# Optimization experiments

Measured on AMD Instinct MI355X. Metric: run time of the kernel, lower is better.

The kernel has to match this reference:

```python
import jax, jax.numpy as jnp
import numpy as np
from jax import lax

N, C_IN, L, K, C_OUT, PAD = 16, 64, 8192, 3, 64, 1

def setup_inputs() -> dict:
    key = jax.random.key(0)
    k1, k2, k3 = jax.random.split(key, 3)
    x = jax.random.normal(k1, (N, C_IN, L), dtype=jnp.float32)
    # kaiming normal (relu): std = sqrt(2 / fan_in), fan_in = C_in * kernel_size
    std_off = np.sqrt(2.0 / (C_IN * K)).astype(np.float32)
    w_off = jax.random.normal(k2, (2 * K, C_IN, K), dtype=jnp.float32) * std_off
    b_off = jnp.zeros((2 * K,), dtype=jnp.float32)
    # 1x1 conv: fan_in = C_in * K (kernel_size 1)
    std_w = np.sqrt(2.0 / (C_IN * K)).astype(np.float32)
    w = jax.random.normal(k3, (C_OUT, C_IN * K), dtype=jnp.float32) * std_w
    b = jnp.zeros((C_OUT,), dtype=jnp.float32)
    return {"x": x, "w_off": w_off, "b_off": b_off, "w": w, "b": b}

def reference(x, w_off, b_off, w, b):
    n, c, l = x.shape
    # offset conv: Conv1d(C, 2K, K, stride=1, padding=PAD)
    offsets = lax.conv_general_dilated(
        x, w_off, window_strides=(1,), padding=[(PAD, PAD)],
        dimension_numbers=("NCH", "OIH", "NCH")) + b_off[None, :, None]
    l_out = offsets.shape[2]
    # [N, 2K, L] -> [N, K, 2, L] -> [N, L, K, 2]; only component 0 is used
    off = offsets.reshape(n, K, 2, l_out).transpose(0, 3, 1, 2)[..., 0]  # [N, L, K]
    x_pad = jnp.pad(x, ((0, 0), (0, 0), (PAD, PAD)))
    lp = l + 2 * PAD
    base = jnp.arange(PAD, lp - PAD, dtype=x.dtype)[None, :, None]  # [1, L, 1]
    grid = jnp.clip(base + off, 0.0, lp - 1)                        # [N, L, K]
    left = jnp.floor(grid).astype(jnp.int32)
    right = jnp.minimum(left + 1, lp - 1)
    alpha = grid - left.astype(x.dtype)                              # [N, L, K]
    idx_l = left.reshape(n, -1)
    idx_r = right.reshape(n, -1)
    gather = jax.vmap(lambda xp, i: xp[:, i])  # per-sample gather over length axis
    x_left = gather(x_pad, idx_l).reshape(n, c, l_out, K)
    x_right = gather(x_pad, idx_r).reshape(n, c, l_out, K)
    a = alpha[:, None]  # [N, 1, L, K]
    x_deform = (1.0 - a) * x_left + a * x_right                      # [N, C, L, K]
    # replicate torch's permute(0,3,2,1).view(N, C*K, L) exactly (row-major)
    x_deform = x_deform.transpose(0, 3, 2, 1).reshape(n, c * K, l_out)
    out = jnp.einsum("om,nml->nol", w, x_deform) + b[None, :, None]
    return out
```

## Files before the change

kernel.cpp:

```cpp
#include <hip/hip_runtime.h>
#include <hip/hip_bf16.h>
#include <math.h>

#define NB   16
#define CIN  64
#define LEN  8192
#define LP2  8195
#define COUT 64
#define MSZ  192

typedef float  f32x4  __attribute__((ext_vector_type(4)));
typedef short  bf16x8 __attribute__((ext_vector_type(8)));

static __device__ inline unsigned short f2bf(float f) {
    __hip_bfloat16 h = __float2bfloat16(f);
    return *reinterpret_cast<unsigned short*>(&h);
}

__global__ __launch_bounds__(256) void prep_kernel(
    const float* __restrict__ x, const float* __restrict__ w_off,
    const float* __restrict__ b_off, const float* __restrict__ w,
    float* __restrict__ gbuf, unsigned int* __restrict__ xt32,
    unsigned short* __restrict__ wtf)
{
    int bid = blockIdx.x;
    int tid = threadIdx.x;

    if (bid >= NB * 128) {
        int b = bid - NB * 128;
        int ot = b / 6, ks = b - ot * 6;
        #pragma unroll
        for (int h = 0; h < 2; ++h) {
            int t2 = tid + h * 256;
            int lq = t2 >> 3, s = t2 & 7;
            int o = ot * 16 + (lq & 15);
            int m = ks * 32 + (lq >> 4) * 8 + s;
            wtf[b * 512 + t2] = f2bf(w[o * MSZ + m]);
        }
        return;
    }

    __shared__ float ps[4][3][64];
    __shared__ unsigned int bt[64 * 33];

    int lane = tid & 63;
    int wid  = __builtin_amdgcn_readfirstlane(tid >> 6);
    int n  = bid >> 7;
    int t  = bid & 127;
    int l0 = t << 6;
    int l  = l0 + lane;
    const float* xn = x + (size_t)n * (CIN * LEN);
    bool okm = (l >= 1);
    bool okp = (l < LEN - 1);

    float a0 = 0.f, a1 = 0.f, a2 = 0.f;
    unsigned int pk[8];

    #pragma unroll
    for (int ci = 0; ci < 16; ci += 2) {
        int c0 = (wid << 4) | ci;
        const float* xc0 = xn + (size_t)c0 * LEN;
        const float* xc1 = xc0 + LEN;
        float xm0 = okm ? xc0[l - 1] : 0.f;
        float x00 = xc0[l];
        float xp0 = okp ? xc0[l + 1] : 0.f;
        float xm1 = okm ? xc1[l - 1] : 0.f;
        float x01 = xc1[l];
        float xp1 = okp ? xc1[l + 1] : 0.f;
        const float* wa = w_off + (size_t)c0 * 3;
        const float* wb = wa + 384;
        const float* wc = wa + 768;
        a0 = fmaf(wa[0], xm0, a0); a0 = fmaf(wa[1], x00, a0); a0 = fmaf(wa[2], xp0, a0);
        a0 = fmaf(wa[3], xm1, a0); a0 = fmaf(wa[4], x01, a0); a0 = fmaf(wa[5], xp1, a0);
        a1 = fmaf(wb[0], xm0, a1); a1 = fmaf(wb[1], x00, a1); a1 = fmaf(wb[2], xp0, a1);
        a1 = fmaf(wb[3], xm1, a1); a1 = fmaf(wb[4], x01, a1); a1 = fmaf(wb[5], xp1, a1);
        a2 = fmaf(wc[0], xm0, a2); a2 = fmaf(wc[1], x00, a2); a2 = fmaf(wc[2], xp0, a2);
        a2 = fmaf(wc[3], xm1, a2); a2 = fmaf(wc[4], x01, a2); a2 = fmaf(wc[5], xp1, a2);
        pk[ci >> 1] = ((unsigned int)f2bf(x01) << 16) | f2bf(x00);
    }

    ps[wid][0][lane] = a0;
    ps[wid][1][lane] = a1;
    ps[wid][2][lane] = a2;
    #pragma unroll
    for (int j = 0; j < 8; ++j)
        bt[lane * 33 + (wid << 3) + j] = pk[j];
    __syncthreads();

    if (tid < 192) {
        int k = tid >> 6, ll = tid & 63;
        float s = b_off[2 * k];
        #pragma unroll
        for (int w4 = 0; w4 < 4; ++w4) s += ps[w4][k][ll];
        float g = fminf(fmaxf((float)(l0 + ll + 1) + s, 0.f), 8193.f);
        gbuf[((size_t)n * LEN + l0 + ll) * 3 + k] = g;
    }

    {
        int row = tid >> 2, grp = tid & 3;
        const unsigned int* src = &bt[row * 33 + (grp << 3)];
        uint4 u0, u1;
        u0.x = src[0]; u0.y = src[1]; u0.z = src[2]; u0.w = src[3];
        u1.x = src[4]; u1.y = src[5]; u1.z = src[6]; u1.w = src[7];
        size_t base = ((size_t)n * LP2 + 1 + l0 + row) * 32 + (grp << 3);
        *(uint4*)&xt32[base]     = u0;
        *(uint4*)&xt32[base + 4] = u1;
    }
    if (t == 0   && tid < 32) xt32[((size_t)n * LP2) * 32 + tid] = 0u;
    if (t == 127 && tid < 64) xt32[((size_t)n * LP2 + 8193 + (tid >> 5)) * 32 + (tid & 31)] = 0u;
}

__global__ __launch_bounds__(256) void dconv6_kernel(
    const unsigned short* __restrict__ xt16, const unsigned short* __restrict__ wtf,
    const float* __restrict__ bias, const float* __restrict__ gbuf,
    float* __restrict__ out)
{
    __shared__ unsigned short Bl[MSZ * 64];
    __shared__ __align__(16) int2 meta[MSZ];
    int tid = threadIdx.x;

    int wg  = blockIdx.x;
    int xcd = wg & 7;
    int tt  = wg >> 3;
    int n   = (xcd << 1) | (tt >> 7);
    int p   = tt & 127;

    if (tid < MSZ) {
        int k = tid >> 6, r = tid & 63;
        int l = (r << 7) | p;
        float g  = gbuf[((size_t)n * LEN + l) * 3 + k];
        float fl = floorf(g);
        meta[tid] = make_int2((int)fl, __float_as_int(g - fl));
    }
    __syncthreads();

    const unsigned short* xb = xt16 + (size_t)n * LP2 * 64;

    #pragma unroll
    for (int j = 0; j < 6; ++j) {
        int task = tid + (j << 8);
        int m  = task >> 3;
        int ch = task & 7;
        int2 mv = meta[m];
        float a = __int_as_float(mv.y);
        const unsigned short* rl = xb + ((size_t)(unsigned)mv.x << 6) + (ch << 3);
        uint4 vl4 = *(const uint4*)rl;
        uint4 vr4 = *(const uint4*)(rl + 64);
        const unsigned int* vl = (const unsigned int*)&vl4;
        const unsigned int* vr = (const unsigned int*)&vr4;
        unsigned int ov[4];
        #pragma unroll
        for (int q = 0; q < 4; ++q) {
            float l0 = __uint_as_float(vl[q] << 16);
            float l1 = __uint_as_float(vl[q] & 0xffff0000u);
            float r0 = __uint_as_float(vr[q] << 16);
            float r1 = __uint_as_float(vr[q] & 0xffff0000u);
            float b0 = fmaf(a, r0 - l0, l0);
            float b1 = fmaf(a, r1 - l1, l1);
            ov[q] = ((unsigned int)f2bf(b1) << 16) | f2bf(b0);
        }
        int dst = (m << 6) + ((ch << 3) ^ (((m >> 3) & 3) << 4));
        *(uint4*)&Bl[dst] = *(const uint4*)ov;
    }
    __syncthreads();

    int lane = tid & 63;
    int ct   = tid >> 6;
    int g4   = lane >> 4;
    int c    = (ct << 4) | (lane & 15);

    f32x4 acc[4] = {};

    #pragma unroll
    for (int ks = 0; ks < 6; ++ks) {
        int mb = ks * 32 + (g4 << 3);
        int cx = c ^ ((((unsigned)(mb >> 3)) & 3) << 4);
        bf16x8 afrag;
        #pragma unroll
        for (int s = 0; s < 8; ++s)
            afrag[s] = (short)Bl[((mb + s) << 6) + cx];

        #pragma unroll
        for (int ot = 0; ot < 4; ++ot) {
            bf16x8 bfrag = *(const bf16x8*)&wtf[(size_t)(((ot * 6 + ks) << 6) + lane) << 3];
            acc[ot] = __builtin_amdgcn_mfma_f32_16x16x32_bf16(afrag, bfrag, acc[ot], 0, 0, 0);
        }
    }

    int q0 = (p << 6) + ct * 16 + g4 * 4;
    #pragma unroll
    for (int ot = 0; ot < 4; ++ot) {
        int o = ot * 16 + (lane & 15);
        float bb = bias[o];
        float4 r4;
        r4.x = acc[ot][0] + bb;
        r4.y = acc[ot][1] + bb;
        r4.z = acc[ot][2] + bb;
        r4.w = acc[ot][3] + bb;
        *(float4*)&out[((size_t)n * COUT + o) * LEN + q0] = r4;
    }
}

extern "C" void kernel_launch(void* const* d_in, const int* in_sizes, int n_in,
                              void* d_out, int out_size, void* d_ws, size_t ws_size,
                              hipStream_t stream) {
    const float* x     = (const float*)d_in[0];
    const float* w_off = (const float*)d_in[1];
    const float* b_off = (const float*)d_in[2];
    const float* w     = (const float*)d_in[3];
    const float* b     = (const float*)d_in[4];
    float* out = (float*)d_out;

    const size_t GBUF_B = (size_t)NB * LEN * 3 * sizeof(float);
    const size_t WTF_B  = (size_t)MSZ * COUT * sizeof(short);
    float*          gbuf = (float*)d_ws;
    unsigned short* wtf  = (unsigned short*)((char*)d_ws + GBUF_B);
    unsigned int*   xt32 = (unsigned int*)((char*)d_ws + GBUF_B + WTF_B);
    unsigned short* xt16 = (unsigned short*)xt32;

    prep_kernel<<<NB * 128 + 24, 256, 0, stream>>>(x, w_off, b_off, w, gbuf, xt32, wtf);
    dconv6_kernel<<<NB * 128, 256, 0, stream>>>(xt16, wtf, b, gbuf, out);
}
```

Measured before the change: 37.44 us.

## Vectorize prep kernel over 256 positions and pipeline gather with MFMA

The prep kernel now has each block handle 256 positions with float4 loads and lane shuffles for the halo, instead of three scalar loads per element. It also writes the transpose with a swizzled layout and vector LDS stores. The main kernel splits the deformable gather into six K-slices with a double-buffered LDS tile, prefetching the next slice's global loads while the current slice is interpolated and fed to MFMA. This cuts LDS footprint and overlaps gather latency with compute, at the cost of extra barriers per slice and fewer prep blocks.

```diff
diff --git a/kernel.cpp b/kernel.cpp
--- a/kernel.cpp
+++ b/kernel.cpp
@@ -17,7 +17,7 @@
     return *reinterpret_cast<unsigned short*>(&h);
 }
 
-__global__ __launch_bounds__(256) void prep_kernel(
+__global__ __launch_bounds__(256) void prep2_kernel(
     const float* __restrict__ x, const float* __restrict__ w_off,
     const float* __restrict__ b_off, const float* __restrict__ w,
     float* __restrict__ gbuf, unsigned int* __restrict__ xt32,
@@ -26,8 +26,8 @@
     int bid = blockIdx.x;
     int tid = threadIdx.x;
 
-    if (bid >= NB * 128) {
-        int b = bid - NB * 128;
+    if (bid >= NB * 32) {
+        int b = bid - NB * 32;
         int ot = b / 6, ks = b - ot * 6;
         #pragma unroll
         for (int h = 0; h < 2; ++h) {
@@ -40,82 +40,107 @@
         return;
     }
 
-    __shared__ float ps[4][3][64];
-    __shared__ unsigned int bt[64 * 33];
+    __shared__ unsigned int bt[256 * 33];
+    __shared__ float ps[4][3][256];
 
     int lane = tid & 63;
     int wid  = __builtin_amdgcn_readfirstlane(tid >> 6);
-    int n  = bid >> 7;
-    int t  = bid & 127;
-    int l0 = t << 6;
-    int l  = l0 + lane;
+    int n  = bid >> 5;
+    int t  = bid & 31;
+    int l0 = t << 8;
+    int lbase = l0 + (lane << 2);
     const float* xn = x + (size_t)n * (CIN * LEN);
-    bool okm = (l >= 1);
-    bool okp = (l < LEN - 1);
-
-    float a0 = 0.f, a1 = 0.f, a2 = 0.f;
-    unsigned int pk[8];
-
-    #pragma unroll
-    for (int ci = 0; ci < 16; ci += 2) {
-        int c0 = (wid << 4) | ci;
+
+    float ak[3][4] = {};
+    unsigned int pk[4][8];
+
+    #pragma unroll
+    for (int pr = 0; pr < 8; ++pr) {
+        int c0 = (wid << 4) + (pr << 1);
         const float* xc0 = xn + (size_t)c0 * LEN;
         const float* xc1 = xc0 + LEN;
-        float xm0 = okm ? xc0[l - 1] : 0.f;
-        float x00 = xc0[l];
-        float xp0 = okp ? xc0[l + 1] : 0.f;
-        float xm1 = okm ? xc1[l - 1] : 0.f;
-        float x01 = xc1[l];
-        float xp1 = okp ? xc1[l + 1] : 0.f;
+        float4 v0 = *(const float4*)&xc0[lbase];
+        float4 v1 = *(const float4*)&xc1[lbase];
+
+        float eL0 = 0.f, eL1 = 0.f, eR0 = 0.f, eR1 = 0.f;
+        if (lane == 0 && l0 > 0)        { eL0 = xc0[l0 - 1];   eL1 = xc1[l0 - 1]; }
+        if (lane == 63 && l0 + 256 < LEN) { eR0 = xc0[l0 + 256]; eR1 = xc1[l0 + 256]; }
+        float pw0 = __shfl_up(v0.w, 1);   if (lane == 0)  pw0 = eL0;
+        float pw1 = __shfl_up(v1.w, 1);   if (lane == 0)  pw1 = eL1;
+        float nx0 = __shfl_down(v0.x, 1); if (lane == 63) nx0 = eR0;
+        float nx1 = __shfl_down(v1.x, 1); if (lane == 63) nx1 = eR1;
+
+        float t0[6] = { pw0, v0.x, v0.y, v0.z, v0.w, nx0 };
+        float t1[6] = { pw1, v1.x, v1.y, v1.z, v1.w, nx1 };
+
         const float* wa = w_off + (size_t)c0 * 3;
         const float* wb = wa + 384;
         const float* wc = wa + 768;
-        a0 = fmaf(wa[0], xm0, a0); a0 = fmaf(wa[1], x00, a0); a0 = fmaf(wa[2], xp0, a0);
-        a0 = fmaf(wa[3], xm1, a0); a0 = fmaf(wa[4], x01, a0); a0 = fmaf(wa[5], xp1, a0);
-        a1 = fmaf(wb[0], xm0, a1); a1 = fmaf(wb[1], x00, a1); a1 = fmaf(wb[2], xp0, a1);
-        a1 = fmaf(wb[3], xm1, a1); a1 = fmaf(wb[4], x01, a1); a1 = fmaf(wb[5], xp1, a1);
-        a2 = fmaf(wc[0], xm0, a2); a2 = fmaf(wc[1], x00, a2); a2 = fmaf(wc[2], xp0, a2);
-        a2 = fmaf(wc[3], xm1, a2); a2 = fmaf(wc[4], x01, a2); a2 = fmaf(wc[5], xp1, a2);
-        pk[ci >> 1] = ((unsigned int)f2bf(x01) << 16) | f2bf(x00);
-    }
-
-    ps[wid][0][lane] = a0;
-    ps[wid][1][lane] = a1;
-    ps[wid][2][lane] = a2;
-    #pragma unroll
-    for (int j = 0; j < 8; ++j)
-        bt[lane * 33 + (wid << 3) + j] = pk[j];
+
+        #pragma unroll
+        for (int li = 0; li < 4; ++li) {
+            float xm0 = t0[li], x00 = t0[li + 1], xp0 = t0[li + 2];
+            float xm1 = t1[li], x01 = t1[li + 1], xp1 = t1[li + 2];
+            float a0 = ak[0][li], a1 = ak[1][li], a2 = ak[2][li];
+            a0 = fmaf(wa[0], xm0, a0); a0 = fmaf(wa[1], x00, a0); a0 = fmaf(wa[2], xp0, a0);
+            a0 = fmaf(wa[3], xm1, a0); a0 = fmaf(wa[4], x01, a0); a0 = fmaf(wa[5], xp1, a0);
+            a1 = fmaf(wb[0], xm0, a1); a1 = fmaf(wb[1], x00, a1); a1 = fmaf(wb[2], xp0, a1);
+            a1 = fmaf(wb[3], xm1, a1); a1 = fmaf(wb[4], x01, a1); a1 = fmaf(wb[5], xp1, a1);
+            a2 = fmaf(wc[0], xm0, a2); a2 = fmaf(wc[1], x00, a2); a2 = fmaf(wc[2], xp0, a2);
+            a2 = fmaf(wc[3], xm1, a2); a2 = fmaf(wc[4], x01, a2); a2 = fmaf(wc[5], xp1, a2);
+            ak[0][li] = a0; ak[1][li] = a1; ak[2][li] = a2;
+            pk[li][pr] = ((unsigned int)f2bf(t1[li + 1]) << 16) | f2bf(t0[li + 1]);
+        }
+    }
+
+    #pragma unroll
+    for (int k = 0; k < 3; ++k)
+        *(float4*)&ps[wid][k][lane << 2] = make_float4(ak[k][0], ak[k][1], ak[k][2], ak[k][3]);
+
+    {
+        int sw = (lane & 3) << 3;
+        int colb = wid << 3;
+        #pragma unroll
+        for (int li = 0; li < 4; ++li) {
+            int row = (lane << 2) + li;
+            *(uint4*)&bt[row * 33 + (colb ^ sw)]       = make_uint4(pk[li][0], pk[li][1], pk[li][2], pk[li][3]);
+            *(uint4*)&bt[row * 33 + ((colb + 4) ^ sw)] = make_uint4(pk[li][4], pk[li][5], pk[li][6], pk[li][7]);
+        }
+    }
     __syncthreads();
 
-    if (tid < 192) {
-        int k = tid >> 6, ll = tid & 63;
-        float s = b_off[2 * k];
-        #pragma unroll
-        for (int w4 = 0; w4 < 4; ++w4) s += ps[w4][k][ll];
-        float g = fminf(fmaxf((float)(l0 + ll + 1) + s, 0.f), 8193.f);
-        gbuf[((size_t)n * LEN + l0 + ll) * 3 + k] = g;
-    }
-
     {
-        int row = tid >> 2, grp = tid & 3;
-        const unsigned int* src = &bt[row * 33 + (grp << 3)];
-        uint4 u0, u1;
-        u0.x = src[0]; u0.y = src[1]; u0.z = src[2]; u0.w = src[3];
-        u1.x = src[4]; u1.y = src[5]; u1.z = src[6]; u1.w = src[7];
-        size_t base = ((size_t)n * LP2 + 1 + l0 + row) * 32 + (grp << 3);
-        *(uint4*)&xt32[base]     = u0;
-        *(uint4*)&xt32[base + 4] = u1;
-    }
-    if (t == 0   && tid < 32) xt32[((size_t)n * LP2) * 32 + tid] = 0u;
-    if (t == 127 && tid < 64) xt32[((size_t)n * LP2 + 8193 + (tid >> 5)) * 32 + (tid & 31)] = 0u;
-}
-
-__global__ __launch_bounds__(256) void dconv6_kernel(
+        int l = tid;
+        #pragma unroll
+        for (int k = 0; k < 3; ++k) {
+            float s = b_off[2 * k];
+            s += ps[0][k][l]; s += ps[1][k][l]; s += ps[2][k][l]; s += ps[3][k][l];
+            float g = fminf(fmaxf((float)(l0 + l + 1) + s, 0.f), 8193.f);
+            gbuf[((size_t)n * LEN + l0 + l) * 3 + k] = g;
+        }
+    }
+
+    #pragma unroll
+    for (int h = 0; h < 4; ++h) {
+        int row = (tid >> 2) + (h << 6);
+        int grp = tid & 3;
+        int sw  = ((row >> 2) & 3) << 3;
+        uint4 u0 = *(const uint4*)&bt[row * 33 + ((grp << 3) ^ sw)];
+        uint4 u1 = *(const uint4*)&bt[row * 33 + (((grp << 3) + 4) ^ sw)];
+        size_t gb = ((size_t)n * LP2 + 1 + l0 + row) * 32 + (grp << 3);
+        *(uint4*)&xt32[gb]     = u0;
+        *(uint4*)&xt32[gb + 4] = u1;
+    }
+    if (t == 0  && tid < 32) xt32[((size_t)n * LP2) * 32 + tid] = 0u;
+    if (t == 31 && tid < 64) xt32[((size_t)n * LP2 + 8193 + (tid >> 5)) * 32 + (tid & 31)] = 0u;
+}
+
+__global__ __launch_bounds__(256) void dconv7_kernel(
     const unsigned short* __restrict__ xt16, const unsigned short* __restrict__ wtf,
     const float* __restrict__ bias, const float* __restrict__ gbuf,
     float* __restrict__ out)
 {
-    __shared__ unsigned short Bl[MSZ * 64];
+    __shared__ unsigned short Bl[2][2048];
     __shared__ __align__(16) int2 meta[MSZ];
     int tid = threadIdx.x;
 
@@ -134,58 +159,65 @@
     }
     __syncthreads();
 
+    int m_loc = tid >> 3, ch = tid & 7;
+    int lane = tid & 63, ct = tid >> 6, g4 = lane >> 4;
+    int c    = (ct << 4) | (lane & 15);
     const unsigned short* xb = xt16 + (size_t)n * LP2 * 64;
 
-    #pragma unroll
-    for (int j = 0; j < 6; ++j) {
-        int task = tid + (j << 8);
-        int m  = task >> 3;
-        int ch = task & 7;
-        int2 mv = meta[m];
-        float a = __int_as_float(mv.y);
-        const unsigned short* rl = xb + ((size_t)(unsigned)mv.x << 6) + (ch << 3);
-        uint4 vl4 = *(const uint4*)rl;
-        uint4 vr4 = *(const uint4*)(rl + 64);
-        const unsigned int* vl = (const unsigned int*)&vl4;
-        const unsigned int* vr = (const unsigned int*)&vr4;
-        unsigned int ov[4];
-        #pragma unroll
-        for (int q = 0; q < 4; ++q) {
-            float l0 = __uint_as_float(vl[q] << 16);
-            float l1 = __uint_as_float(vl[q] & 0xffff0000u);
-            float r0 = __uint_as_float(vr[q] << 16);
-            float r1 = __uint_as_float(vr[q] & 0xffff0000u);
-            float b0 = fmaf(a, r0 - l0, l0);
-            float b1 = fmaf(a, r1 - l1, l1);
-            ov[q] = ((unsigned int)f2bf(b1) << 16) | f2bf(b0);
-        }
-        int dst = (m << 6) + ((ch << 3) ^ (((m >> 3) & 3) << 4));
-        *(uint4*)&Bl[dst] = *(const uint4*)ov;
-    }
-    __syncthreads();
-
-    int lane = tid & 63;
-    int ct   = tid >> 6;
-    int g4   = lane >> 4;
-    int c    = (ct << 4) | (lane & 15);
+    int dst = (m_loc << 6) + ((ch << 3) ^ (((m_loc >> 3) & 3) << 4));
+    int cxr = c ^ ((g4 & 3) << 4);
+
+    uint4 vlA, vrA, vlB, vrB;
+    float aA, aB;
+
+    #define GISS(KS, VL, VR, AL) do {                                        \
+        int2 mv = meta[(KS) * 32 + m_loc];                                   \
+        AL = __int_as_float(mv.y);                                           \
+        const unsigned short* rl = xb + ((size_t)(unsigned)mv.x << 6) + (ch << 3); \
+        VL = *(const uint4*)rl;                                              \
+        VR = *(const uint4*)(rl + 64);                                       \
+    } while (0)
+
+    GISS(0, vlA, vrA, aA);
 
     f32x4 acc[4] = {};
 
     #pragma unroll
     for (int ks = 0; ks < 6; ++ks) {
-        int mb = ks * 32 + (g4 << 3);
-        int cx = c ^ ((((unsigned)(mb >> 3)) & 3) << 4);
+        if (ks < 5) GISS(ks + 1, vlB, vrB, aB);
+
+        {
+            const unsigned int* vl = (const unsigned int*)&vlA;
+            const unsigned int* vr = (const unsigned int*)&vrA;
+            unsigned int ov[4];
+            #pragma unroll
+            for (int q = 0; q < 4; ++q) {
+                float l0v = __uint_as_float(vl[q] << 16);
+                float l1v = __uint_as_float(vl[q] & 0xffff0000u);
+                float r0v = __uint_as_float(vr[q] << 16);
+                float r1v = __uint_as_float(vr[q] & 0xffff0000u);
+                float b0 = fmaf(aA, r0v - l0v, l0v);
+                float b1 = fmaf(aA, r1v - l1v, l1v);
+                ov[q] = ((unsigned int)f2bf(b1) << 16) | f2bf(b0);
+            }
+            *(uint4*)&Bl[ks & 1][dst] = *(const uint4*)ov;
+        }
+        __syncthreads();
+
         bf16x8 afrag;
         #pragma unroll
         for (int s = 0; s < 8; ++s)
-            afrag[s] = (short)Bl[((mb + s) << 6) + cx];
+            afrag[s] = (short)Bl[ks & 1][(((g4 << 3) + s) << 6) + cxr];
 
         #pragma unroll
         for (int ot = 0; ot < 4; ++ot) {
             bf16x8 bfrag = *(const bf16x8*)&wtf[(size_t)(((ot * 6 + ks) << 6) + lane) << 3];
             acc[ot] = __builtin_amdgcn_mfma_f32_16x16x32_bf16(afrag, bfrag, acc[ot], 0, 0, 0);
         }
-    }
+
+        if (ks < 5) { vlA = vlB; vrA = vrB; aA = aB; }
+    }
+    #undef GISS
 
     int q0 = (p << 6) + ct * 16 + g4 * 4;
     #pragma unroll
@@ -218,6 +250,6 @@
     unsigned int*   xt32 = (unsigned int*)((char*)d_ws + GBUF_B + WTF_B);
     unsigned short* xt16 = (unsigned short*)xt32;
 
-    prep_kernel<<<NB * 128 + 24, 256, 0, stream>>>(x, w_off, b_off, w, gbuf, xt32, wtf);
-    dconv6_kernel<<<NB * 128, 256, 0, stream>>>(xt16, wtf, b, gbuf, out);
-}
+    prep2_kernel<<<NB * 32 + 24, 256, 0, stream>>>(x, w_off, b_off, w, gbuf, xt32, wtf);
+    dconv7_kernel<<<NB * 128, 256, 0, stream>>>(xt16, wtf, b, gbuf, out);
+}
```

New measurement: 43.27 us. 15.6% more time.
